# Performance work log

Hardware: AMD Instinct MI355X
Metric: run time of the kernel (lower is better)

Reference implementation:

```python
import jax, jax.numpy as jnp
import numpy as np

B, F, N, D, P = 32, 32, 36, 2048, 512  # batch, frames, objects, input dim, projected dim


def setup_inputs() -> dict:
    key = jax.random.key(0)
    ks = jax.random.split(key, 8)
    s = 1.0 / np.sqrt(D).astype(np.float32)  # torch nn.Linear default init range
    u = lambda k, shape: jax.random.uniform(k, shape, jnp.float32, -s, s)
    return {
        "object_variable": jax.random.normal(ks[0], (B, F, N, D), jnp.float32),
        "W_proj": u(ks[1], (D, P)), "b_proj": u(ks[2], (P,)),
        "W_sigma": u(ks[3], (D, P)), "b_sigma": u(ks[4], (P,)),
        "W_psi": u(ks[5], (D, P)), "b_psi": u(ks[6], (P,)),
        "W_r": u(ks[7], (D, P)),  # bias=False
    }


def reference(object_variable, W_proj, b_proj, W_sigma, b_sigma, W_psi, b_psi, W_r):
    # Dropouts are identity in eval mode.
    x = object_variable                                   # [B,F,N,D]
    r_feat = x @ W_proj + b_proj                          # [B,F,N,P]
    sig = x @ W_sigma + b_sigma                           # [B,F,N,P]
    psi = x @ W_psi + b_psi                               # [B,F,N,P]
    a_coeff = jnp.einsum('bfnp,bfmp->bfnm', sig, psi)     # [B,F,N,N] unscaled QK^T
    a_hat = jax.nn.softmax(a_coeff, axis=-1)
    r_hat = jnp.einsum('bfnm,bfmp->bfnp', a_hat, x @ W_r) # AV matmul
    return (r_feat, r_hat)
```

## Files before the change

kernel.cpp:

```cpp
#include <hip/hip_runtime.h>
#include <hip/hip_fp16.h>
#include <stdint.h>

typedef _Float16 half2v __attribute__((ext_vector_type(2)));
typedef _Float16 half4v __attribute__((ext_vector_type(4)));
typedef _Float16 half8v __attribute__((ext_vector_type(8)));
typedef float    float4v __attribute__((ext_vector_type(4)));

#define KDIM 2048
#define PDIM 512
#define MROWS 36864
#define NOBJ 36
#define NTOT 2048

__device__ __forceinline__ void gload_lds16(const void* g, void* l) {
    using gptr_t = const __attribute__((address_space(1))) unsigned int*;
    using lptr_t = __attribute__((address_space(3))) unsigned int*;
    __builtin_amdgcn_global_load_lds((gptr_t)(uintptr_t)g,
                                     (lptr_t)(uint32_t)(uintptr_t)l,
                                     16, 0, 0);
}

__global__ __launch_bounds__(256)
void cvt_x_kernel(const float* __restrict__ x, _Float16* __restrict__ xh) {
    const size_t i = ((size_t)blockIdx.x * 256 + threadIdx.x) * 8;
    float4v a = *(const float4v*)&x[i];
    float4v b = *(const float4v*)&x[i + 4];
    half8v h;
    h[0] = (_Float16)a[0]; h[1] = (_Float16)a[1];
    h[2] = (_Float16)a[2]; h[3] = (_Float16)a[3];
    h[4] = (_Float16)b[0]; h[5] = (_Float16)b[1];
    h[6] = (_Float16)b[2]; h[7] = (_Float16)b[3];
    *(half8v*)&xh[i] = h;
}

__global__ __launch_bounds__(256)
void cvt_w_kernel(const float* __restrict__ Wp, const float* __restrict__ Ws,
                  const float* __restrict__ Wq, const float* __restrict__ Wr,
                  _Float16* __restrict__ wt) {
    const int bid = blockIdx.x;
    const int mat = bid >> 10;
    const int t   = bid & 1023;
    const int kt  = t >> 4;
    const int pt  = t & 15;
    const float* W = (mat == 0) ? Wp : (mat == 1) ? Ws : (mat == 2) ? Wq : Wr;

    __shared__ float tile[32][33];
    const int tx = threadIdx.x & 31;
    const int ty = threadIdx.x >> 5;
    #pragma unroll
    for (int r = 0; r < 4; ++r) {
        const int k = kt * 32 + ty + r * 8;
        tile[ty + r * 8][tx] = W[(size_t)k * PDIM + pt * 32 + tx];
    }
    __syncthreads();
    #pragma unroll
    for (int r = 0; r < 4; ++r) {
        const int p = pt * 32 + ty + r * 8;
        const int n = mat * PDIM + p;
        wt[(size_t)n * KDIM + kt * 32 + tx] = (_Float16)tile[tx][ty + r * 8];
    }
}

__global__ __launch_bounds__(256, 2)
void proj_gemm(const _Float16* __restrict__ A, const _Float16* __restrict__ Bt,
               float* __restrict__ rfeat, _Float16* __restrict__ sg,
               _Float16* __restrict__ ph, _Float16* __restrict__ vh,
               const float* __restrict__ bp, const float* __restrict__ bs,
               const float* __restrict__ bq) {
    __shared__ _Float16 sA[128 * 32];
    __shared__ _Float16 sB[128 * 32];

    const int tid  = threadIdx.x;
    const int lane = tid & 63;
    const int wave = tid >> 6;

    const int n0 = (blockIdx.x & 15) * 128;
    const int m0 = (blockIdx.x >> 4) * 128;

    const int srow = tid >> 2;
    const int skc  = (tid & 3) * 8;
    const _Float16* ga0 = A  + (size_t)(m0 + srow) * KDIM + skc;
    const _Float16* ga1 = A  + (size_t)(m0 + 64 + srow) * KDIM + skc;
    const _Float16* gb0 = Bt + (size_t)(n0 + srow) * KDIM + skc;
    const _Float16* gb1 = Bt + (size_t)(n0 + 64 + srow) * KDIM + skc;

    char* lA = (char*)sA + tid * 16;
    char* lB = (char*)sB + tid * 16;

    const int m_off = (wave >> 1) * 64;
    const int n_off = (wave & 1) * 64;
    const int frow  = lane & 15;
    const int fk    = (lane >> 4) * 8;

    float4v acc[4][4] = {};

    for (int kt = 0; kt < KDIM / 32; ++kt) {
        __syncthreads();
        gload_lds16(ga0, lA);
        gload_lds16(ga1, lA + 4096);
        gload_lds16(gb0, lB);
        gload_lds16(gb1, lB + 4096);
        ga0 += 32; ga1 += 32; gb0 += 32; gb1 += 32;
        __syncthreads();

        half8v af[4], bf[4];
        #pragma unroll
        for (int i = 0; i < 4; ++i)
            af[i] = *(const half8v*)&sA[(m_off + i * 16 + frow) * 32 + fk];
        #pragma unroll
        for (int j = 0; j < 4; ++j)
            bf[j] = *(const half8v*)&sB[(n_off + j * 16 + frow) * 32 + fk];
        #pragma unroll
        for (int i = 0; i < 4; ++i)
            #pragma unroll
            for (int j = 0; j < 4; ++j)
                acc[i][j] = __builtin_amdgcn_mfma_f32_16x16x32_f16(af[i], bf[j], acc[i][j], 0, 0, 0);
    }

    const int seg = n0 >> 9;
    const int pn0 = (n0 & 511) + n_off;
    #pragma unroll
    for (int j = 0; j < 4; ++j) {
        const int pcol = pn0 + j * 16 + frow;
        float bias = 0.0f;
        if (seg == 0)      bias = bp[pcol];
        else if (seg == 1) bias = bs[pcol];
        else if (seg == 2) bias = bq[pcol];
        #pragma unroll
        for (int i = 0; i < 4; ++i) {
            const int rb = m0 + m_off + i * 16 + (lane >> 4) * 4;
            #pragma unroll
            for (int r = 0; r < 4; ++r) {
                const float val = acc[i][j][r] + bias;
                const size_t off = (size_t)(rb + r) * PDIM + pcol;
                if (seg == 0)      rfeat[off] = val;
                else if (seg == 1) sg[off] = (_Float16)val;
                else if (seg == 2) ph[off] = (_Float16)val;
                else               vh[off] = (_Float16)val;
            }
        }
    }
}

__global__ __launch_bounds__(256, 2)
void attn_kernel(const _Float16* __restrict__ sg, const _Float16* __restrict__ ph,
                 const _Float16* __restrict__ vh, float* __restrict__ rhat) {
    __shared__ _Float16 ss[NOBJ * 520];
    __shared__ _Float16 ps[NOBJ * 520];
    __shared__ float    Ls[NOBJ * 37];

    const int tid = threadIdx.x;
    const size_t base = (size_t)blockIdx.x * (NOBJ * PDIM);

    for (int c = tid; c < (NOBJ * PDIM / 8); c += 256) {
        const int row = c >> 6;
        const int col = (c & 63) * 8;
        *(half8v*)&ss[row * 520 + col] = *(const half8v*)&sg[base + row * PDIM + col];
        *(half8v*)&ps[row * 520 + col] = *(const half8v*)&ph[base + row * PDIM + col];
    }
    __syncthreads();

    if (tid < 144) {
        const int i0 = (tid / 12) * 3;
        const int j0 = (tid % 12) * 3;
        float accv[3][3] = {};
        for (int p = 0; p < PDIM; p += 8) {
            half8v si[3], pj[3];
            #pragma unroll
            for (int ii = 0; ii < 3; ++ii) si[ii] = *(const half8v*)&ss[(i0 + ii) * 520 + p];
            #pragma unroll
            for (int jj = 0; jj < 3; ++jj) pj[jj] = *(const half8v*)&ps[(j0 + jj) * 520 + p];
            #pragma unroll
            for (int ii = 0; ii < 3; ++ii)
                #pragma unroll
                for (int jj = 0; jj < 3; ++jj) {
                    float t = accv[ii][jj];
                    #pragma unroll
                    for (int q = 0; q < 4; ++q) {
                        half2v x2; x2[0] = si[ii][2 * q]; x2[1] = si[ii][2 * q + 1];
                        half2v y2; y2[0] = pj[jj][2 * q]; y2[1] = pj[jj][2 * q + 1];
                        t = __builtin_amdgcn_fdot2(x2, y2, t, false);
                    }
                    accv[ii][jj] = t;
                }
        }
        #pragma unroll
        for (int ii = 0; ii < 3; ++ii)
            #pragma unroll
            for (int jj = 0; jj < 3; ++jj)
                Ls[(i0 + ii) * 37 + (j0 + jj)] = accv[ii][jj];
    }
    __syncthreads();

    if (tid < NOBJ) {
        float mx = -1e30f;
        for (int j = 0; j < NOBJ; ++j) mx = fmaxf(mx, Ls[tid * 37 + j]);
        float sum = 0.0f;
        for (int j = 0; j < NOBJ; ++j) {
            float e = __expf(Ls[tid * 37 + j] - mx);
            sum += e;
            Ls[tid * 37 + j] = e;
        }
        const float inv = 1.0f / sum;
        for (int j = 0; j < NOBJ; ++j) Ls[tid * 37 + j] *= inv;
    }
    __syncthreads();

    const int p4 = (tid & 127) * 4;
    const int r0 = tid >> 7;
    float4v acc[18] = {};
    for (int j = 0; j < NOBJ; ++j) {
        half4v v4 = *(const half4v*)&vh[base + (size_t)j * PDIM + p4];
        float4v vf;
        vf[0] = (float)v4[0]; vf[1] = (float)v4[1];
        vf[2] = (float)v4[2]; vf[3] = (float)v4[3];
        #pragma unroll
        for (int m = 0; m < 18; ++m) {
            const float aw = Ls[(2 * m + r0) * 37 + j];
            acc[m] += aw * vf;
        }
    }
    #pragma unroll
    for (int m = 0; m < 18; ++m)
        *(float4v*)&rhat[base + (size_t)(2 * m + r0) * PDIM + p4] = acc[m];
}

extern "C" void kernel_launch(void* const* d_in, const int* in_sizes, int n_in,
                              void* d_out, int out_size, void* d_ws, size_t ws_size,
                              hipStream_t stream) {
    const float* x   = (const float*)d_in[0];
    const float* Wp  = (const float*)d_in[1];
    const float* bp  = (const float*)d_in[2];
    const float* Wsg = (const float*)d_in[3];
    const float* bsg = (const float*)d_in[4];
    const float* Wps = (const float*)d_in[5];
    const float* bps = (const float*)d_in[6];
    const float* Wr  = (const float*)d_in[7];
    float* out = (float*)d_out;

    char* ws = (char*)d_ws;
    _Float16* xh = (_Float16*)(ws);
    _Float16* wt = (_Float16*)(ws + 150994944UL);
    _Float16* sg = (_Float16*)(ws + 159383552UL);
    _Float16* ph = (_Float16*)(ws + 197132288UL);
    _Float16* vh = (_Float16*)(ws + 234881024UL);

    cvt_x_kernel<<<36864, 256, 0, stream>>>(x, xh);
    cvt_w_kernel<<<4096, 256, 0, stream>>>(Wp, Wsg, Wps, Wr, wt);
    proj_gemm<<<288 * 16, 256, 0, stream>>>(xh, wt, out, sg, ph, vh, bp, bsg, bps);
    attn_kernel<<<1024, 256, 0, stream>>>(sg, ph, vh, out + 18874368);
}
```

Before: 907.6 us.

## Fuse fp32-to-fp16 conversion of X into projection GEMM with register prefetch

```diff
diff --git a/kernel.cpp b/kernel.cpp
--- a/kernel.cpp
+++ b/kernel.cpp
@@ -19,19 +19,6 @@
     __builtin_amdgcn_global_load_lds((gptr_t)(uintptr_t)g,
                                      (lptr_t)(uint32_t)(uintptr_t)l,
                                      16, 0, 0);
-}
-
-__global__ __launch_bounds__(256)
-void cvt_x_kernel(const float* __restrict__ x, _Float16* __restrict__ xh) {
-    const size_t i = ((size_t)blockIdx.x * 256 + threadIdx.x) * 8;
-    float4v a = *(const float4v*)&x[i];
-    float4v b = *(const float4v*)&x[i + 4];
-    half8v h;
-    h[0] = (_Float16)a[0]; h[1] = (_Float16)a[1];
-    h[2] = (_Float16)a[2]; h[3] = (_Float16)a[3];
-    h[4] = (_Float16)b[0]; h[5] = (_Float16)b[1];
-    h[6] = (_Float16)b[2]; h[7] = (_Float16)b[3];
-    *(half8v*)&xh[i] = h;
 }
 
 __global__ __launch_bounds__(256)
@@ -63,59 +50,89 @@
 }
 
 __global__ __launch_bounds__(256, 2)
-void proj_gemm(const _Float16* __restrict__ A, const _Float16* __restrict__ Bt,
+void proj_gemm(const float* __restrict__ X, const _Float16* __restrict__ Bt,
                float* __restrict__ rfeat, _Float16* __restrict__ sg,
                _Float16* __restrict__ ph, _Float16* __restrict__ vh,
                const float* __restrict__ bp, const float* __restrict__ bs,
                const float* __restrict__ bq) {
-    __shared__ _Float16 sA[128 * 32];
-    __shared__ _Float16 sB[128 * 32];
+    __shared__ _Float16 sA[512 * 8];
+    __shared__ _Float16 sB[512 * 8];
 
     const int tid  = threadIdx.x;
     const int lane = tid & 63;
     const int wave = tid >> 6;
 
-    const int n0 = (blockIdx.x & 15) * 128;
-    const int m0 = (blockIdx.x >> 4) * 128;
-
-    const int srow = tid >> 2;
-    const int skc  = (tid & 3) * 8;
-    const _Float16* ga0 = A  + (size_t)(m0 + srow) * KDIM + skc;
-    const _Float16* ga1 = A  + (size_t)(m0 + 64 + srow) * KDIM + skc;
-    const _Float16* gb0 = Bt + (size_t)(n0 + srow) * KDIM + skc;
-    const _Float16* gb1 = Bt + (size_t)(n0 + 64 + srow) * KDIM + skc;
-
-    char* lA = (char*)sA + tid * 16;
-    char* lB = (char*)sB + tid * 16;
+    const int xcd = blockIdx.x & 7;
+    const int idx = blockIdx.x >> 3;
+    const int m0  = (xcd * 36 + (idx >> 4)) * 128;
+    const int n0  = (idx & 15) * 128;
+
+    const int srow = tid & 127;
+    const int skc0 = tid >> 7;
+    const _Float16* gb0 = Bt + (size_t)(n0 + srow) * KDIM + skc0 * 8;
+    const _Float16* gb1 = gb0 + 16;
+    const float* gx0 = X + (size_t)(m0 + srow) * KDIM + skc0 * 8;
+    const float* gx1 = gx0 + 16;
+
+    char* lB0 = (char*)sB + tid * 16;
+    char* lB1 = (char*)sB + (tid + 256) * 16;
 
     const int m_off = (wave >> 1) * 64;
     const int n_off = (wave & 1) * 64;
     const int frow  = lane & 15;
-    const int fk    = (lane >> 4) * 8;
+    const int fchunk = lane >> 4;
 
     float4v acc[4][4] = {};
+
+    float4v a0 = *(const float4v*)gx0;
+    float4v a1 = *(const float4v*)(gx0 + 4);
+    float4v a2 = *(const float4v*)gx1;
+    float4v a3 = *(const float4v*)(gx1 + 4);
 
     for (int kt = 0; kt < KDIM / 32; ++kt) {
         __syncthreads();
-        gload_lds16(ga0, lA);
-        gload_lds16(ga1, lA + 4096);
-        gload_lds16(gb0, lB);
-        gload_lds16(gb1, lB + 4096);
-        ga0 += 32; ga1 += 32; gb0 += 32; gb1 += 32;
+
+        float4v p0, p1, p2, p3;
+        if (kt < KDIM / 32 - 1) {
+            gx0 += 32; gx1 += 32;
+            p0 = *(const float4v*)gx0;
+            p1 = *(const float4v*)(gx0 + 4);
+            p2 = *(const float4v*)gx1;
+            p3 = *(const float4v*)(gx1 + 4);
+        }
+
+        gload_lds16(gb0, lB0);
+        gload_lds16(gb1, lB1);
+        gb0 += 32; gb1 += 32;
+
+        half8v h0, h1;
+        h0[0] = (_Float16)a0[0]; h0[1] = (_Float16)a0[1];
+        h0[2] = (_Float16)a0[2]; h0[3] = (_Float16)a0[3];
+        h0[4] = (_Float16)a1[0]; h0[5] = (_Float16)a1[1];
+        h0[6] = (_Float16)a1[2]; h0[7] = (_Float16)a1[3];
+        h1[0] = (_Float16)a2[0]; h1[1] = (_Float16)a2[1];
+        h1[2] = (_Float16)a2[2]; h1[3] = (_Float16)a2[3];
+        h1[4] = (_Float16)a3[0]; h1[5] = (_Float16)a3[1];
+        h1[6] = (_Float16)a3[2]; h1[7] = (_Float16)a3[3];
+        *(half8v*)&sA[(size_t)tid * 8] = h0;
+        *(half8v*)&sA[(size_t)(tid + 256) * 8] = h1;
+
         __syncthreads();
 
         half8v af[4], bf[4];
         #pragma unroll
         for (int i = 0; i < 4; ++i)
-            af[i] = *(const half8v*)&sA[(m_off + i * 16 + frow) * 32 + fk];
+            af[i] = *(const half8v*)&sA[(fchunk * 128 + m_off + i * 16 + frow) * 8];
         #pragma unroll
         for (int j = 0; j < 4; ++j)
-            bf[j] = *(const half8v*)&sB[(n_off + j * 16 + frow) * 32 + fk];
+            bf[j] = *(const half8v*)&sB[(fchunk * 128 + n_off + j * 16 + frow) * 8];
         #pragma unroll
         for (int i = 0; i < 4; ++i)
             #pragma unroll
             for (int j = 0; j < 4; ++j)
                 acc[i][j] = __builtin_amdgcn_mfma_f32_16x16x32_f16(af[i], bf[j], acc[i][j], 0, 0, 0);
+
+        if (kt < KDIM / 32 - 1) { a0 = p0; a1 = p1; a2 = p2; a3 = p3; }
     }
 
     const int seg = n0 >> 9;
@@ -240,14 +257,12 @@
     float* out = (float*)d_out;
 
     char* ws = (char*)d_ws;
-    _Float16* xh = (_Float16*)(ws);
-    _Float16* wt = (_Float16*)(ws + 150994944UL);
-    _Float16* sg = (_Float16*)(ws + 159383552UL);
-    _Float16* ph = (_Float16*)(ws + 197132288UL);
-    _Float16* vh = (_Float16*)(ws + 234881024UL);
-
-    cvt_x_kernel<<<36864, 256, 0, stream>>>(x, xh);
+    _Float16* wt = (_Float16*)(ws);
+    _Float16* sg = (_Float16*)(ws + 8388608UL);
+    _Float16* ph = (_Float16*)(ws + 46137344UL);
+    _Float16* vh = (_Float16*)(ws + 83886080UL);
+
     cvt_w_kernel<<<4096, 256, 0, stream>>>(Wp, Wsg, Wps, Wr, wt);
-    proj_gemm<<<288 * 16, 256, 0, stream>>>(xh, wt, out, sg, ph, vh, bp, bsg, bps);
+    proj_gemm<<<288 * 16, 256, 0, stream>>>(x, wt, out, sg, ph, vh, bp, bsg, bps);
     attn_kernel<<<1024, 256, 0, stream>>>(sg, ph, vh, out + 18874368);
 }
```

After: 1.338 ms. 1.47x slower.
